# Kernel optimization log

Hardware: AMD Instinct MI355X
Metric: run time of the kernel (lower is better)

## Reference

```python
import jax, jax.numpy as jnp
import numpy as np
from jax import lax

IMG = 512            # image H = W
FH = FW = 32         # feature map spatial size
A = 9                # anchors per location (3 sizes x 3 ratios)
N = FH * FW * A      # total anchors = 9216
IOU_THR = 0.7
MIN_SCORE = 0.5
MIN_SIZE = 1e-3


def make_anchors():
    """Anchors in centroid format (cx, cy, w, h), ordered (H, W, A)."""
    stride = IMG / FH
    sizes = np.array([32.0, 64.0, 128.0])
    ratios = np.array([0.5, 1.0, 2.0])
    ws = (sizes[:, None] / np.sqrt(ratios)[None, :]).reshape(-1)  # (A,)
    hs = (sizes[:, None] * np.sqrt(ratios)[None, :]).reshape(-1)  # (A,)
    cx = (np.arange(FW) + 0.5) * stride
    cy = (np.arange(FH) + 0.5) * stride
    CX = np.broadcast_to(cx[None, :, None], (FH, FW, A))
    CY = np.broadcast_to(cy[:, None, None], (FH, FW, A))
    Wg = np.broadcast_to(ws[None, None, :], (FH, FW, A))
    Hg = np.broadcast_to(hs[None, None, :], (FH, FW, A))
    anc = np.stack([CX, CY, Wg, Hg], axis=-1).reshape(-1, 4)
    return jnp.asarray(anc, dtype=jnp.float32)


def pairwise_iou(b):
    # b: (N,4) corners x1,y1,x2,y2
    x1, y1, x2, y2 = b[:, 0], b[:, 1], b[:, 2], b[:, 3]
    area = (x2 - x1) * (y2 - y1)
    ix1 = jnp.maximum(x1[:, None], x1[None, :])
    iy1 = jnp.maximum(y1[:, None], y1[None, :])
    ix2 = jnp.minimum(x2[:, None], x2[None, :])
    iy2 = jnp.minimum(y2[:, None], y2[None, :])
    inter = jnp.maximum(ix2 - ix1, 0.0) * jnp.maximum(iy2 - iy1, 0.0)
    union = area[:, None] + area[None, :] - inter
    return inter / jnp.maximum(union, 1e-9)


def nms_keep(boxes, scores, valid):
    """Greedy NMS. Returns bool keep mask of shape (N,). Index decisions only."""
    s = jnp.where(valid, scores, -jnp.inf)
    order = jnp.argsort(-s)
    b = boxes[order]
    v = valid[order]
    ious = pairwise_iou(b)  # (N, N)
    idx = jnp.arange(N)

    def body(i, supp):
        keep_i = (~supp[i]) & v[i]
        return supp | (keep_i & (ious[i] > IOU_THR) & (idx > i))

    supp = lax.fori_loop(0, N, body, jnp.zeros(N, dtype=bool))
    keep_sorted = (~supp) & v
    return jnp.zeros(N, dtype=bool).at[order].set(keep_sorted)


def setup_inputs() -> dict:
    key = jax.random.key(0)
    ks = jax.random.split(key, 4)
    return {
        "feature_map": jax.random.normal(ks[0], (1, 256, FH, FW), jnp.float32),
        "conv1_w": jax.random.normal(ks[1], (512, 256, 3, 3), jnp.float32) * 0.02,
        "conv1_b": jnp.zeros((512,), jnp.float32),
        "conv2_w": jax.random.normal(ks[2], (A, 512), jnp.float32) * 0.01,
        "conv2_b": jnp.zeros((A,), jnp.float32),
        "conv3_w": jax.random.normal(ks[3], (4 * A, 512), jnp.float32) * 0.01,
        "conv3_b": jnp.zeros((4 * A,), jnp.float32),
    }


def reference(feature_map, conv1_w, conv1_b, conv2_w, conv2_b, conv3_w, conv3_b):
    anchors = make_anchors()  # (N,4) cx,cy,w,h

    # --- conv backbone head ---
    h = lax.conv_general_dilated(
        feature_map, conv1_w, (1, 1), "SAME",
        dimension_numbers=("NCHW", "OIHW", "NCHW"))
    h = jax.nn.relu(h + conv1_b[None, :, None, None])  # (1,512,H,W)

    scores = jax.nn.sigmoid(
        jnp.einsum("bchw,ac->bahw", h, conv2_w) + conv2_b[None, :, None, None])
    scores = scores.transpose(0, 2, 3, 1).reshape(-1)  # (N,) ordered (H,W,A)

    off = jnp.einsum("bchw,oc->bohw", h, conv3_w) + conv3_b[None, :, None, None]
    off = off.reshape(1, A, 4, FH, FW).transpose(0, 3, 4, 1, 2).reshape(-1, 4)

    acx, acy, aw, ah = anchors[:, 0], anchors[:, 1], anchors[:, 2], anchors[:, 3]
    cx = acx + off[:, 0] * aw
    cy = acy + off[:, 1] * ah
    bw = aw * jnp.exp(off[:, 2])
    bh = ah * jnp.exp(off[:, 3])
    boxes = jnp.stack([cx - bw / 2, cy - bh / 2, cx + bw / 2, cy + bh / 2], axis=1)

    # --- clip to image ---
    lo = jnp.array([0.0, 0.0, 0.0, 0.0], jnp.float32)
    hi = jnp.array([IMG, IMG, IMG, IMG], jnp.float32)
    boxes = jnp.clip(boxes, lo, hi)

    # --- remove small boxes + score threshold (as a mask, jit-safe) ---
    valid = ((boxes[:, 2] - boxes[:, 0]) >= MIN_SIZE) \
          & ((boxes[:, 3] - boxes[:, 1]) >= MIN_SIZE) \
          & (scores >= MIN_SCORE)

    # --- NMS (selection is index-based; no gradient through the decision) ---
    keep = nms_keep(lax.stop_gradient(boxes), lax.stop_gradient(scores), valid)

    out = jnp.concatenate(
        [boxes * keep[:, None].astype(boxes.dtype),
         (scores * keep.astype(scores.dtype))[:, None]], axis=1)  # (N,5)
    return out
```

## Files before the change

### kernel.cpp

```cpp
#include <hip/hip_runtime.h>
#include <math.h>

#define FHW   32
#define NA    9
#define NBOX  9216
#define C1    256
#define C2    512
#define KTOT  2304
#define KS    8
#define KCH   (KTOT / KS)
#define CAP   64
#define ECAP  16384
#define ROUNDS 96

struct AnchorWH { float w[NA]; float h[NA]; };

#define FP_OFF    0u
#define WT_OFF    1183744u
#define HP_OFF    5902336u
#define BOX_OFF   22679552u
#define SC_OFF    22827008u
#define VL_OFF    22863872u
#define DEG_OFF   22900736u
#define ADJ_OFF   22937600u
#define KEEP_OFF  24117248u
#define NV_OFF    24154112u

__global__ __launch_bounds__(256) void k_prep(const float* __restrict__ fin,
                                              float* __restrict__ Fp,
                                              unsigned int* __restrict__ deg,
                                              unsigned int* __restrict__ keepG,
                                              unsigned int* __restrict__ nv,
                                              const float* __restrict__ w1,
                                              float* __restrict__ Wt) {
    if (blockIdx.x < 1156) {
        int idx = blockIdx.x * 256 + threadIdx.x;
        if (idx < 256 * 34 * 34) {
            int c   = idx / 1156;
            int rem = idx - c * 1156;
            int yy  = rem / 34;
            int xx  = rem - yy * 34;
            float v = 0.f;
            if (yy >= 1 && yy <= 32 && xx >= 1 && xx <= 32)
                v = fin[c * 1024 + (yy - 1) * 32 + (xx - 1)];
            Fp[idx] = v;
        }
        if (idx < NBOX) { deg[idx] = 0u; keepG[idx] = 0u; }
        if (idx == 0)   *nv = 0u;
    } else {
        __shared__ float tile[32][33];
        int tb  = blockIdx.x - 1156;
        int k0  = (tb % 72) * 32;
        int oc0 = (tb / 72) * 32;
        int t   = threadIdx.x;
        int r0 = t >> 5, c = t & 31;
        #pragma unroll
        for (int i = 0; i < 4; ++i) {
            int r = r0 + 8 * i;
            tile[r][c] = w1[(oc0 + r) * KTOT + k0 + c];
        }
        __syncthreads();
        #pragma unroll
        for (int i = 0; i < 4; ++i) {
            int kk = r0 + 8 * i;
            Wt[(k0 + kk) * C2 + oc0 + c] = tile[c][kk];
        }
    }
}

__global__ __launch_bounds__(256, 2) void k_gemm(const float* __restrict__ Fp,
                                                 const float* __restrict__ Wt,
                                                 float* __restrict__ hp) {
    const int id = blockIdx.x;
    const int bx = id >> 5, g = id & 31;
    const int by = g >> 3, kz = g & 7;
    const int p0  = bx * 64;
    const int oc0 = by * 128;
    const int k0b = kz * KCH;
    const int t  = threadIdx.x;
    const int ty = t >> 4, tx = t & 15;

    __shared__ float As[16][64];
    __shared__ float Bs[16][128];

    float acc[4][8];
    #pragma unroll
    for (int r = 0; r < 4; ++r)
        #pragma unroll
        for (int c = 0; c < 8; ++c) acc[r][c] = 0.f;

    for (int kt = 0; kt < KCH; kt += 16) {
        #pragma unroll
        for (int i = 0; i < 4; ++i) {
            int e  = t + 256 * i;
            int kk = e >> 6, pp = e & 63;
            int k   = k0b + kt + kk;
            int c   = k / 9;
            int kap = k - c * 9;
            int dy  = kap / 3;
            int dx  = kap - dy * 3;
            int p  = p0 + pp;
            int y  = p >> 5, x = p & 31;
            As[kk][pp] = Fp[(c * 34 + y + dy) * 34 + x + dx];
        }
        #pragma unroll
        for (int i = 0; i < 2; ++i) {
            int e4 = t + 256 * i;
            int kk = e4 >> 5, c4 = e4 & 31;
            *(float4*)&Bs[kk][c4 * 4] =
                *(const float4*)&Wt[(k0b + kt + kk) * C2 + oc0 + c4 * 4];
        }
        __syncthreads();
        #pragma unroll
        for (int kk = 0; kk < 16; ++kk) {
            float a[4], b[8];
            *(float4*)&a[0] = *(const float4*)&As[kk][ty * 4];
            *(float4*)&b[0] = *(const float4*)&Bs[kk][tx * 4];
            *(float4*)&b[4] = *(const float4*)&Bs[kk][tx * 4 + 64];
            #pragma unroll
            for (int r = 0; r < 4; ++r)
                #pragma unroll
                for (int c = 0; c < 8; ++c) acc[r][c] += a[r] * b[c];
        }
        __syncthreads();
    }
    #pragma unroll
    for (int r = 0; r < 4; ++r) {
        int p = p0 + ty * 4 + r;
        float* dst = hp + ((kz * 1024 + p) * C2 + oc0 + tx * 4);
        *(float4*)dst        = *(float4*)&acc[r][0];
        *(float4*)(dst + 64) = *(float4*)&acc[r][4];
    }
}

__global__ __launch_bounds__(256) void k_heads(const float* __restrict__ hp,
                                               const float* __restrict__ b1,
                                               const float* __restrict__ w2,
                                               const float* __restrict__ b2,
                                               const float* __restrict__ w3,
                                               const float* __restrict__ b3,
                                               float* __restrict__ boxes,
                                               float* __restrict__ scoresG,
                                               unsigned int* __restrict__ nv,
                                               unsigned int* __restrict__ vlist,
                                               AnchorWH awh) {
    const int p0 = blockIdx.x * 4;
    const int t  = threadIdx.x;
    __shared__ float hrow[4][C2];
    __shared__ float arr[4][45];

    #pragma unroll
    for (int px = 0; px < 4; ++px) {
        int p = p0 + px;
        #pragma unroll
        for (int i = 0; i < 2; ++i) {
            int c = t + 256 * i;
            float s = b1[c];
            #pragma unroll
            for (int ks = 0; ks < KS; ++ks) s += hp[(ks * 1024 + p) * C2 + c];
            hrow[px][c] = fmaxf(s, 0.f);
        }
    }
    __syncthreads();

    const int w = t >> 6, lane = t & 63;
    for (int job = w; job < 180; job += 4) {
        int px = job / 45, j = job - px * 45;
        const float* wp = (j < 9) ? (w2 + j * C2) : (w3 + (j - 9) * C2);
        float s = 0.f;
        #pragma unroll
        for (int i = 0; i < 8; ++i) s += hrow[px][lane + 64 * i] * wp[lane + 64 * i];
        #pragma unroll
        for (int d = 1; d < 64; d <<= 1) s += __shfl_xor(s, d, 64);
        if (lane == 0) arr[px][j] = s;
    }
    __syncthreads();

    if (t < 36) {
        int px = t / 9, a = t - px * 9;
        int p = p0 + px;
        float logit = arr[px][a] + b2[a];
        float score = 1.f / (1.f + expf(-logit));
        float o0 = arr[px][9 + a * 4 + 0] + b3[a * 4 + 0];
        float o1 = arr[px][9 + a * 4 + 1] + b3[a * 4 + 1];
        float o2 = arr[px][9 + a * 4 + 2] + b3[a * 4 + 2];
        float o3 = arr[px][9 + a * 4 + 3] + b3[a * 4 + 3];
        int y = p >> 5, x = p & 31;
        float ax = (x + 0.5f) * 16.f, ay = (y + 0.5f) * 16.f;
        float aw = awh.w[a], ah = awh.h[a];
        float cx = ax + o0 * aw;
        float cy = ay + o1 * ah;
        float bw = aw * expf(o2);
        float bh = ah * expf(o3);
        float x1 = fminf(fmaxf(cx - bw * 0.5f, 0.f), 512.f);
        float y1 = fminf(fmaxf(cy - bh * 0.5f, 0.f), 512.f);
        float x2 = fminf(fmaxf(cx + bw * 0.5f, 0.f), 512.f);
        float y2 = fminf(fmaxf(cy + bh * 0.5f, 0.f), 512.f);
        int n = p * 9 + a;
        float4 bx4; bx4.x = x1; bx4.y = y1; bx4.z = x2; bx4.w = y2;
        ((float4*)boxes)[n] = bx4;
        scoresG[n] = score;
        bool valid = (x2 - x1 >= 0.001f) && (y2 - y1 >= 0.001f) && (score >= 0.5f);
        if (valid) {
            unsigned int ci = atomicAdd(nv, 1u);
            vlist[ci] = (unsigned int)n;
        }
    }
}

__global__ __launch_bounds__(256) void k_adj(const unsigned int* __restrict__ nvp,
                                             const unsigned int* __restrict__ vlist,
                                             const float* __restrict__ boxes,
                                             const float* __restrict__ scoresG,
                                             unsigned int* __restrict__ deg,
                                             unsigned short* __restrict__ adj) {
    const int Nv = (int)*nvp;
    int b = blockIdx.x;
    int tv = (int)(sqrtf(2.f * b + 0.25f) - 0.5f);
    while ((tv + 1) * (tv + 2) / 2 <= b) tv++;
    while (tv * (tv + 1) / 2 > b) tv--;
    int tu = b - tv * (tv + 1) / 2;
    if (tv * 128 >= Nv) return;

    __shared__ float4 ub[128], vb[128];
    __shared__ float  us[128], vs[128];
    __shared__ int    uo[128], vo[128];
    int t = threadIdx.x;
    if (t < 128) {
        int gi = tu * 128 + t;
        if (gi < Nv) { int n = (int)vlist[gi]; ub[t] = ((const float4*)boxes)[n]; us[t] = scoresG[n]; uo[t] = n; }
        else us[t] = -1.f;
    } else {
        int tt = t - 128;
        int gj = tv * 128 + tt;
        if (gj < Nv) { int n = (int)vlist[gj]; vb[tt] = ((const float4*)boxes)[n]; vs[tt] = scoresG[n]; vo[tt] = n; }
        else vs[tt] = -1.f;
    }
    __syncthreads();

    for (int s = 0; s < 64; ++s) {
        int q  = t + 256 * s;
        int i  = q >> 7, jj = q & 127;
        if (tu == tv && i >= jj) continue;
        float su = us[i], sv = vs[jj];
        if (su < 0.f || sv < 0.f) continue;
        float4 bu = ub[i], bv = vb[jj];
        float au = (bu.z - bu.x) * (bu.w - bu.y);
        float av = (bv.z - bv.x) * (bv.w - bv.y);
        float ix1 = fmaxf(bu.x, bv.x), iy1 = fmaxf(bu.y, bv.y);
        float ix2 = fminf(bu.z, bv.z), iy2 = fminf(bu.w, bv.w);
        float inter = fmaxf(ix2 - ix1, 0.f) * fmaxf(iy2 - iy1, 0.f);
        float uni = au + av - inter;
        float iou = inter / fmaxf(uni, 1e-9f);
        if (iou > 0.7f) {
            int gi = tu * 128 + i, gj = tv * 128 + jj;
            bool uHigh = (su > sv) || (su == sv && uo[i] < vo[jj]);
            int lower = uHigh ? gj : gi;
            int upper = uHigh ? gi : gj;
            unsigned int slot = atomicAdd(&deg[lower], 1u);
            if (slot < CAP) adj[lower * CAP + slot] = (unsigned short)upper;
        }
    }
}

__global__ __launch_bounds__(512) void k_peel(const unsigned int* __restrict__ nvp,
                                              const unsigned int* __restrict__ vlist,
                                              const unsigned int* __restrict__ degG,
                                              const unsigned short* __restrict__ adjG,
                                              unsigned int* __restrict__ keepG) {
    __shared__ unsigned short offL[NBOX + 2];
    __shared__ unsigned char  st[NBOX];
    __shared__ unsigned short csr[ECAP];
    __shared__ unsigned int   scratch[512];
    __shared__ unsigned char  flags[ROUNDS];
    const int t  = threadIdx.x;
    const int Nv = (int)*nvp;
    const int chunk = (Nv + 511) / 512;
    const int i0 = t * chunk;
    const int i1 = (i0 + chunk < Nv) ? (i0 + chunk) : Nv;

    if (t < ROUNDS) flags[t] = 0;

    unsigned int lsum = 0;
    for (int i = i0; i < i1; ++i) {
        unsigned int d = degG[i];
        if (d > CAP) d = CAP;
        st[i] = (unsigned char)d;
        lsum += d;
    }
    scratch[t] = lsum;
    __syncthreads();
    for (int ofs = 1; ofs < 512; ofs <<= 1) {
        unsigned int v = (t >= ofs) ? scratch[t - ofs] : 0u;
        __syncthreads();
        scratch[t] += v;
        __syncthreads();
    }
    if (t == 511) {
        unsigned int tot = scratch[511];
        offL[Nv] = (unsigned short)(tot < ECAP ? tot : ECAP);
    }
    unsigned int amask = 0;
    {
        unsigned int off = scratch[t] - lsum;
        for (int i = i0; i < i1; ++i) {
            unsigned int o = (off < ECAP) ? off : ECAP;
            offL[i] = (unsigned short)o;
            int d = st[i];
            int ld = (int)ECAP - (int)o; if (ld > d) ld = d; if (ld < 0) ld = 0;
            for (int s = 0; s < ld; ++s)
                csr[o + s] = adjG[i * CAP + s];
            off += d;
            if (d == 0) st[i] = 1;
            else { st[i] = 0; amask |= 1u << (i - i0); }
        }
    }
    __syncthreads();

    for (int r = 0; r < ROUNDS; ++r) {
        bool any = false;
        unsigned int m = amask;
        while (m) {
            int b = __ffs(m) - 1; m &= m - 1;
            int i = i0 + b;
            int o = offL[i], on = offL[i + 1];
            int d, ld;
            if (on < ECAP) { d = on - o; ld = d; }
            else {
                unsigned int dg = degG[i]; d = (dg > CAP) ? CAP : (int)dg;
                ld = (int)ECAP - o; if (ld < 0) ld = 0; if (ld > d) ld = d;
            }
            bool kseen = false, useen = false;
            for (int s = 0; s < d; ++s) {
                int j = (s < ld) ? (int)csr[o + s] : (int)adjG[i * CAP + s];
                unsigned char v = st[j];
                kseen |= (v == 1);
                useen |= (v == 0);
            }
            if (kseen)       { st[i] = 2; any = true; amask &= ~(1u << b); }
            else if (!useen) { st[i] = 1; any = true; amask &= ~(1u << b); }
        }
        if (any) flags[r] = 1;
        __syncthreads();
        if (!flags[r]) break;
    }

    for (int i = i0; i < i1; ++i)
        if (st[i] == 1) keepG[vlist[i]] = 1u;
}

__global__ __launch_bounds__(256) void k_out(const float* __restrict__ boxes,
                                             const float* __restrict__ scoresG,
                                             const unsigned int* __restrict__ keepG,
                                             float* __restrict__ out) {
    int n = blockIdx.x * 256 + threadIdx.x;
    if (n >= NBOX) return;
    float k = keepG[n] ? 1.f : 0.f;
    float4 b = ((const float4*)boxes)[n];
    out[n * 5 + 0] = b.x * k;
    out[n * 5 + 1] = b.y * k;
    out[n * 5 + 2] = b.z * k;
    out[n * 5 + 3] = b.w * k;
    out[n * 5 + 4] = scoresG[n] * k;
}

extern "C" void kernel_launch(void* const* d_in, const int* in_sizes, int n_in,
                              void* d_out, int out_size, void* d_ws, size_t ws_size,
                              hipStream_t stream) {
    const float* fin = (const float*)d_in[0];
    const float* w1  = (const float*)d_in[1];
    const float* b1  = (const float*)d_in[2];
    const float* w2  = (const float*)d_in[3];
    const float* b2  = (const float*)d_in[4];
    const float* w3  = (const float*)d_in[5];
    const float* b3  = (const float*)d_in[6];
    float* out = (float*)d_out;

    char* ws = (char*)d_ws;
    float*          Fp    = (float*)(ws + FP_OFF);
    float*          Wt    = (float*)(ws + WT_OFF);
    float*          hp    = (float*)(ws + HP_OFF);
    float*          boxes = (float*)(ws + BOX_OFF);
    float*          sc    = (float*)(ws + SC_OFF);
    unsigned int*   vlist = (unsigned int*)(ws + VL_OFF);
    unsigned int*   deg   = (unsigned int*)(ws + DEG_OFF);
    unsigned short* adj   = (unsigned short*)(ws + ADJ_OFF);
    unsigned int*   keepG = (unsigned int*)(ws + KEEP_OFF);
    unsigned int*   nv    = (unsigned int*)(ws + NV_OFF);

    AnchorWH awh;
    {
        const double sizes[3]  = {32.0, 64.0, 128.0};
        const double ratios[3] = {0.5, 1.0, 2.0};
        for (int si = 0; si < 3; ++si)
            for (int ri = 0; ri < 3; ++ri) {
                awh.w[si * 3 + ri] = (float)(sizes[si] / sqrt(ratios[ri]));
                awh.h[si * 3 + ri] = (float)(sizes[si] * sqrt(ratios[ri]));
            }
    }

    k_prep<<<dim3(1156 + 72 * 16), 256, 0, stream>>>(fin, Fp, deg, keepG, nv, w1, Wt);
    k_gemm<<<dim3(512), 256, 0, stream>>>(Fp, Wt, hp);
    k_heads<<<dim3(256), 256, 0, stream>>>(hp, b1, w2, b2, w3, b3, boxes, sc, nv, vlist, awh);
    k_adj<<<dim3(72 * 73 / 2), 256, 0, stream>>>(nv, vlist, boxes, sc, deg, adj);
    k_peel<<<dim3(1), 512, 0, stream>>>(nv, vlist, deg, adj, keepG);
    k_out<<<dim3((NBOX + 255) / 256), 256, 0, stream>>>(boxes, sc, keepG, out);
}
```

Measured before the change: 203.7 us.

## Add 16-way split-K GEMM with 8x8 register tiles and register prefetch

Adds a new conv-GEMM variant that splits K into 16 chunks, uses 128-thread blocks with 8x8 per-thread accumulators, and prefetches the next A/B tiles into registers while computing the current one. It is selected only when the workspace is large enough for 16 partial-sum slices. The workspace layout is reordered so the partial-sum buffer sits last, and the heads kernel takes the split count at runtime. The goal is more blocks and more latency hiding in the GEMM. The cost is twice the partial-sum write and read traffic in the heads reduction, plus higher register pressure.

```diff
diff --git a/kernel.cpp b/kernel.cpp
--- a/kernel.cpp
+++ b/kernel.cpp
@@ -7,8 +7,10 @@
 #define C1    256
 #define C2    512
 #define KTOT  2304
-#define KS    8
-#define KCH   (KTOT / KS)
+#define KS8   8
+#define KCH8  288
+#define KS16  16
+#define KCH16 144
 #define CAP   64
 #define ECAP  16384
 #define ROUNDS 96
@@ -17,14 +19,15 @@
 
 #define FP_OFF    0u
 #define WT_OFF    1183744u
-#define HP_OFF    5902336u
-#define BOX_OFF   22679552u
-#define SC_OFF    22827008u
-#define VL_OFF    22863872u
-#define DEG_OFF   22900736u
-#define ADJ_OFF   22937600u
-#define KEEP_OFF  24117248u
-#define NV_OFF    24154112u
+#define BOX_OFF   5902336u
+#define SC_OFF    6049792u
+#define VL_OFF    6086656u
+#define DEG_OFF   6123520u
+#define KEEP_OFF  6160384u
+#define NV_OFF    6197248u
+#define ADJ_OFF   6197504u
+#define HP_OFF    7377152u
+#define WS_NEED16 (HP_OFF + (size_t)KS16 * 1024 * 512 * 4)
 
 __global__ __launch_bounds__(256) void k_prep(const float* __restrict__ fin,
                                               float* __restrict__ Fp,
@@ -68,15 +71,111 @@
     }
 }
 
-__global__ __launch_bounds__(256, 2) void k_gemm(const float* __restrict__ Fp,
-                                                 const float* __restrict__ Wt,
-                                                 float* __restrict__ hp) {
+__global__ __launch_bounds__(128, 2) void k_gemm16(const float* __restrict__ Fp,
+                                                   const float* __restrict__ Wt,
+                                                   float* __restrict__ hp) {
+    const int id = blockIdx.x;
+    const int bx = id >> 6, g = id & 63;
+    const int by = g >> 4, kz = g & 15;
+    const int p0 = bx * 64, oc0 = by * 128, k0b = kz * KCH16;
+    const int t  = threadIdx.x;
+    const int ty = t >> 4, tx = t & 15;
+
+    __shared__ float As[16][64];
+    __shared__ float Bs[16][128];
+
+    float acc[8][8];
+    #pragma unroll
+    for (int r = 0; r < 8; ++r)
+        #pragma unroll
+        for (int c = 0; c < 8; ++c) acc[r][c] = 0.f;
+
+    float  pa[8];
+    float4 pb[4];
+
+    #pragma unroll
+    for (int i = 0; i < 8; ++i) {
+        int e = t + 128 * i;
+        int kk = e >> 6, pp = e & 63;
+        int k = k0b + kk;
+        int c = k / 9;
+        int kap = k - c * 9;
+        int dy = kap / 3, dx = kap - dy * 3;
+        int p = p0 + pp;
+        int y = p >> 5, x = p & 31;
+        pa[i] = Fp[(c * 34 + y + dy) * 34 + x + dx];
+    }
+    #pragma unroll
+    for (int i = 0; i < 4; ++i) {
+        int e4 = t + 128 * i;
+        int kk = e4 >> 5, c4 = e4 & 31;
+        pb[i] = *(const float4*)&Wt[(k0b + kk) * C2 + oc0 + c4 * 4];
+    }
+
+    for (int kt = 0; kt < KCH16; kt += 16) {
+        #pragma unroll
+        for (int i = 0; i < 8; ++i) {
+            int e = t + 128 * i;
+            As[e >> 6][e & 63] = pa[i];
+        }
+        #pragma unroll
+        for (int i = 0; i < 4; ++i) {
+            int e4 = t + 128 * i;
+            *(float4*)&Bs[e4 >> 5][(e4 & 31) * 4] = pb[i];
+        }
+        __syncthreads();
+        if (kt + 16 < KCH16) {
+            #pragma unroll
+            for (int i = 0; i < 8; ++i) {
+                int e = t + 128 * i;
+                int kk = e >> 6, pp = e & 63;
+                int k = k0b + kt + 16 + kk;
+                int c = k / 9;
+                int kap = k - c * 9;
+                int dy = kap / 3, dx = kap - dy * 3;
+                int p = p0 + pp;
+                int y = p >> 5, x = p & 31;
+                pa[i] = Fp[(c * 34 + y + dy) * 34 + x + dx];
+            }
+            #pragma unroll
+            for (int i = 0; i < 4; ++i) {
+                int e4 = t + 128 * i;
+                int kk = e4 >> 5, c4 = e4 & 31;
+                pb[i] = *(const float4*)&Wt[(k0b + kt + 16 + kk) * C2 + oc0 + c4 * 4];
+            }
+        }
+        #pragma unroll
+        for (int kk = 0; kk < 16; ++kk) {
+            float a[8], b[8];
+            *(float4*)&a[0] = *(const float4*)&As[kk][ty * 4];
+            *(float4*)&a[4] = *(const float4*)&As[kk][ty * 4 + 32];
+            *(float4*)&b[0] = *(const float4*)&Bs[kk][tx * 4];
+            *(float4*)&b[4] = *(const float4*)&Bs[kk][tx * 4 + 64];
+            #pragma unroll
+            for (int r = 0; r < 8; ++r)
+                #pragma unroll
+                for (int c = 0; c < 8; ++c) acc[r][c] += a[r] * b[c];
+        }
+        __syncthreads();
+    }
+    #pragma unroll
+    for (int r = 0; r < 8; ++r) {
+        int p = p0 + ty * 4 + (r & 3) + 32 * (r >> 2);
+        float* dst = hp + ((kz * 1024 + p) * C2 + oc0 + tx * 4);
+        *(float4*)dst        = *(float4*)&acc[r][0];
+        *(float4*)(dst + 64) = *(float4*)&acc[r][4];
+    }
+}
+
+__global__ __launch_bounds__(256, 2) void k_gemm8(const float* __restrict__ Fp,
+                                                  const float* __restrict__ Wt,
+                                                  float* __restrict__ hp) {
     const int id = blockIdx.x;
     const int bx = id >> 5, g = id & 31;
     const int by = g >> 3, kz = g & 7;
     const int p0  = bx * 64;
     const int oc0 = by * 128;
-    const int k0b = kz * KCH;
+    const int k0b = kz * KCH8;
     const int t  = threadIdx.x;
     const int ty = t >> 4, tx = t & 15;
 
@@ -89,7 +188,7 @@
         #pragma unroll
         for (int c = 0; c < 8; ++c) acc[r][c] = 0.f;
 
-    for (int kt = 0; kt < KCH; kt += 16) {
+    for (int kt = 0; kt < KCH8; kt += 16) {
         #pragma unroll
         for (int i = 0; i < 4; ++i) {
             int e  = t + 256 * i;
@@ -143,7 +242,7 @@
                                                float* __restrict__ scoresG,
                                                unsigned int* __restrict__ nv,
                                                unsigned int* __restrict__ vlist,
-                                               AnchorWH awh) {
+                                               AnchorWH awh, int KSdyn) {
     const int p0 = blockIdx.x * 4;
     const int t  = threadIdx.x;
     __shared__ float hrow[4][C2];
@@ -156,8 +255,8 @@
         for (int i = 0; i < 2; ++i) {
             int c = t + 256 * i;
             float s = b1[c];
-            #pragma unroll
-            for (int ks = 0; ks < KS; ++ks) s += hp[(ks * 1024 + p) * C2 + c];
+            #pragma unroll 4
+            for (int ks = 0; ks < KSdyn; ++ks) s += hp[(ks * 1024 + p) * C2 + c];
             hrow[px][c] = fmaxf(s, 0.f);
         }
     }
@@ -379,14 +478,17 @@
     char* ws = (char*)d_ws;
     float*          Fp    = (float*)(ws + FP_OFF);
     float*          Wt    = (float*)(ws + WT_OFF);
-    float*          hp    = (float*)(ws + HP_OFF);
     float*          boxes = (float*)(ws + BOX_OFF);
     float*          sc    = (float*)(ws + SC_OFF);
     unsigned int*   vlist = (unsigned int*)(ws + VL_OFF);
     unsigned int*   deg   = (unsigned int*)(ws + DEG_OFF);
-    unsigned short* adj   = (unsigned short*)(ws + ADJ_OFF);
     unsigned int*   keepG = (unsigned int*)(ws + KEEP_OFF);
     unsigned int*   nv    = (unsigned int*)(ws + NV_OFF);
+    unsigned short* adj   = (unsigned short*)(ws + ADJ_OFF);
+    float*          hp    = (float*)(ws + HP_OFF);
+
+    const bool big = (ws_size >= WS_NEED16);
+    const int  KSdyn = big ? KS16 : KS8;
 
     AnchorWH awh;
     {
@@ -400,8 +502,9 @@
     }
 
     k_prep<<<dim3(1156 + 72 * 16), 256, 0, stream>>>(fin, Fp, deg, keepG, nv, w1, Wt);
-    k_gemm<<<dim3(512), 256, 0, stream>>>(Fp, Wt, hp);
-    k_heads<<<dim3(256), 256, 0, stream>>>(hp, b1, w2, b2, w3, b3, boxes, sc, nv, vlist, awh);
+    if (big) k_gemm16<<<dim3(1024), 128, 0, stream>>>(Fp, Wt, hp);
+    else     k_gemm8 <<<dim3(512),  256, 0, stream>>>(Fp, Wt, hp);
+    k_heads<<<dim3(256), 256, 0, stream>>>(hp, b1, w2, b2, w3, b3, boxes, sc, nv, vlist, awh, KSdyn);
     k_adj<<<dim3(72 * 73 / 2), 256, 0, stream>>>(nv, vlist, boxes, sc, deg, adj);
     k_peel<<<dim3(1), 512, 0, stream>>>(nv, vlist, deg, adj, keepG);
     k_out<<<dim3((NBOX + 255) / 256), 256, 0, stream>>>(boxes, sc, keepG, out);
```

Result: slower. 226.0 us (+10.9%).

## Fuse all stages into one persistent kernel with software grid barriers

Applied to the files above, without the earlier changes.

Replaces six separate launches with a single persistent kernel of 512 blocks that moves between stages using an atomic-counter grid barrier. The heads stage now covers 2 pixels per block, the adjacency stage loops over dynamically sized tiles based on the valid count, and peel runs on block 0 with 256 threads and 64-bit active masks. The intent is to remove launch and inter-kernel gaps. In exchange it relies on all 512 blocks being co-resident, shrinks the shared CSR capacity, and the single-block peel stage now has half the threads.

```diff
diff --git a/kernel.cpp b/kernel.cpp
--- a/kernel.cpp
+++ b/kernel.cpp
@@ -8,360 +8,377 @@
 #define C2    512
 #define KTOT  2304
 #define KS    8
-#define KCH   (KTOT / KS)
+#define KCH   288
 #define CAP   64
-#define ECAP  16384
+#define ECAP  12288
 #define ROUNDS 96
+#define NBLK  512
 
 struct AnchorWH { float w[NA]; float h[NA]; };
 
 #define FP_OFF    0u
 #define WT_OFF    1183744u
-#define HP_OFF    5902336u
-#define BOX_OFF   22679552u
-#define SC_OFF    22827008u
-#define VL_OFF    22863872u
-#define DEG_OFF   22900736u
-#define ADJ_OFF   22937600u
-#define KEEP_OFF  24117248u
-#define NV_OFF    24154112u
-
-__global__ __launch_bounds__(256) void k_prep(const float* __restrict__ fin,
-                                              float* __restrict__ Fp,
-                                              unsigned int* __restrict__ deg,
-                                              unsigned int* __restrict__ keepG,
-                                              unsigned int* __restrict__ nv,
-                                              const float* __restrict__ w1,
-                                              float* __restrict__ Wt) {
-    if (blockIdx.x < 1156) {
-        int idx = blockIdx.x * 256 + threadIdx.x;
-        if (idx < 256 * 34 * 34) {
-            int c   = idx / 1156;
-            int rem = idx - c * 1156;
-            int yy  = rem / 34;
-            int xx  = rem - yy * 34;
-            float v = 0.f;
-            if (yy >= 1 && yy <= 32 && xx >= 1 && xx <= 32)
-                v = fin[c * 1024 + (yy - 1) * 32 + (xx - 1)];
-            Fp[idx] = v;
-        }
-        if (idx < NBOX) { deg[idx] = 0u; keepG[idx] = 0u; }
-        if (idx == 0)   *nv = 0u;
-    } else {
-        __shared__ float tile[32][33];
-        int tb  = blockIdx.x - 1156;
-        int k0  = (tb % 72) * 32;
-        int oc0 = (tb / 72) * 32;
-        int t   = threadIdx.x;
-        int r0 = t >> 5, c = t & 31;
+#define BOX_OFF   5902336u
+#define SC_OFF    6049792u
+#define VL_OFF    6086656u
+#define DEG_OFF   6123520u
+#define KEEP_OFF  6160384u
+#define NV_OFF    6197248u
+#define BAR_OFF   6197376u
+#define ADJ_OFF   6197504u
+#define HP_OFF    7377152u
+
+struct SmemPrep  { float tile[32][33]; };
+struct SmemGemm  { float As[16][64]; float Bs[16][128]; };
+struct SmemHeads { float hrow[2][C2]; float arr[2][45]; };
+struct SmemAdj   { float4 ub[128]; float4 vb[128]; float us[128]; float vs[128]; int uo[128]; int vo[128]; };
+struct SmemPeel  {
+    unsigned short offL[NBOX + 2];
+    unsigned char  st[NBOX];
+    unsigned short csr[ECAP];
+    unsigned int   scratch[256];
+    unsigned char  flags[ROUNDS];
+};
+union SmemU { SmemPrep p; SmemGemm g; SmemHeads h; SmemAdj a; SmemPeel e; };
+
+__device__ __forceinline__ void gbar(unsigned int* cnt, unsigned int phase) {
+    __syncthreads();
+    if (threadIdx.x == 0) {
+        __threadfence();
+        atomicAdd(cnt, 1u);
+        const unsigned int target = NBLK * phase;
+        while (atomicAdd(cnt, 0u) < target)
+            __builtin_amdgcn_s_sleep(15);
+        __threadfence();
+    }
+    __syncthreads();
+}
+
+__global__ __launch_bounds__(256, 2) void k_all(const float* __restrict__ fin,
+                                                const float* __restrict__ w1,
+                                                const float* __restrict__ b1,
+                                                const float* __restrict__ w2,
+                                                const float* __restrict__ b2,
+                                                const float* __restrict__ w3,
+                                                const float* __restrict__ b3,
+                                                float* __restrict__ out,
+                                                char* __restrict__ ws,
+                                                AnchorWH awh) {
+    __shared__ SmemU sm;
+
+    float*          Fp    = (float*)(ws + FP_OFF);
+    float*          Wt    = (float*)(ws + WT_OFF);
+    float*          boxes = (float*)(ws + BOX_OFF);
+    float*          sc    = (float*)(ws + SC_OFF);
+    unsigned int*   vlist = (unsigned int*)(ws + VL_OFF);
+    unsigned int*   deg   = (unsigned int*)(ws + DEG_OFF);
+    unsigned int*   keepG = (unsigned int*)(ws + KEEP_OFF);
+    unsigned int*   nvp   = (unsigned int*)(ws + NV_OFF);
+    unsigned int*   bar   = (unsigned int*)(ws + BAR_OFF);
+    unsigned short* adjG  = (unsigned short*)(ws + ADJ_OFF);
+    float*          hp    = (float*)(ws + HP_OFF);
+
+    const int t   = threadIdx.x;
+    const int gid = blockIdx.x * 256 + t;
+
+    for (int idx = gid; idx < 256 * 34 * 34; idx += NBLK * 256) {
+        int c   = idx / 1156;
+        int rem = idx - c * 1156;
+        int yy  = rem / 34;
+        int xx  = rem - yy * 34;
+        float v = 0.f;
+        if (yy >= 1 && yy <= 32 && xx >= 1 && xx <= 32)
+            v = fin[c * 1024 + (yy - 1) * 32 + (xx - 1)];
+        Fp[idx] = v;
+    }
+    if (gid < NBOX) { deg[gid] = 0u; keepG[gid] = 0u; }
+    if (gid == 0)   *nvp = 0u;
+    {
+        const int r0 = t >> 5, c = t & 31;
+        for (int tb = blockIdx.x; tb < 1152; tb += NBLK) {
+            int k0  = (tb % 72) * 32;
+            int oc0 = (tb / 72) * 32;
+            #pragma unroll
+            for (int i = 0; i < 4; ++i) {
+                int r = r0 + 8 * i;
+                sm.p.tile[r][c] = w1[(oc0 + r) * KTOT + k0 + c];
+            }
+            __syncthreads();
+            #pragma unroll
+            for (int i = 0; i < 4; ++i) {
+                int kk = r0 + 8 * i;
+                Wt[(k0 + kk) * C2 + oc0 + c] = sm.p.tile[c][kk];
+            }
+            __syncthreads();
+        }
+    }
+    gbar(bar, 1);
+
+    {
+        const int id = blockIdx.x;
+        const int bx = id >> 5, g = id & 31;
+        const int by = g >> 3, kz = g & 7;
+        const int p0  = bx * 64;
+        const int oc0 = by * 128;
+        const int k0b = kz * KCH;
+        const int ty = t >> 4, tx = t & 15;
+
+        float acc[4][8];
         #pragma unroll
-        for (int i = 0; i < 4; ++i) {
-            int r = r0 + 8 * i;
-            tile[r][c] = w1[(oc0 + r) * KTOT + k0 + c];
+        for (int r = 0; r < 4; ++r)
+            #pragma unroll
+            for (int c = 0; c < 8; ++c) acc[r][c] = 0.f;
+
+        for (int kt = 0; kt < KCH; kt += 16) {
+            #pragma unroll
+            for (int i = 0; i < 4; ++i) {
+                int e  = t + 256 * i;
+                int kk = e >> 6, pp = e & 63;
+                int k   = k0b + kt + kk;
+                int c   = k / 9;
+                int kap = k - c * 9;
+                int dy  = kap / 3;
+                int dx  = kap - dy * 3;
+                int p  = p0 + pp;
+                int y  = p >> 5, x = p & 31;
+                sm.g.As[kk][pp] = Fp[(c * 34 + y + dy) * 34 + x + dx];
+            }
+            #pragma unroll
+            for (int i = 0; i < 2; ++i) {
+                int e4 = t + 256 * i;
+                int kk = e4 >> 5, c4 = e4 & 31;
+                *(float4*)&sm.g.Bs[kk][c4 * 4] =
+                    *(const float4*)&Wt[(k0b + kt + kk) * C2 + oc0 + c4 * 4];
+            }
+            __syncthreads();
+            #pragma unroll
+            for (int kk = 0; kk < 16; ++kk) {
+                float a[4], b[8];
+                *(float4*)&a[0] = *(const float4*)&sm.g.As[kk][ty * 4];
+                *(float4*)&b[0] = *(const float4*)&sm.g.Bs[kk][tx * 4];
+                *(float4*)&b[4] = *(const float4*)&sm.g.Bs[kk][tx * 4 + 64];
+                #pragma unroll
+                for (int r = 0; r < 4; ++r)
+                    #pragma unroll
+                    for (int c = 0; c < 8; ++c) acc[r][c] += a[r] * b[c];
+            }
+            __syncthreads();
+        }
+        #pragma unroll
+        for (int r = 0; r < 4; ++r) {
+            int p = p0 + ty * 4 + r;
+            float* dst = hp + ((kz * 1024 + p) * C2 + oc0 + tx * 4);
+            *(float4*)dst        = *(float4*)&acc[r][0];
+            *(float4*)(dst + 64) = *(float4*)&acc[r][4];
+        }
+    }
+    gbar(bar, 2);
+
+    {
+        const int p0 = blockIdx.x * 2;
+        #pragma unroll
+        for (int px = 0; px < 2; ++px) {
+            int p = p0 + px;
+            #pragma unroll
+            for (int i = 0; i < 2; ++i) {
+                int c = t + 256 * i;
+                float s = b1[c];
+                #pragma unroll
+                for (int ks = 0; ks < KS; ++ks) s += hp[(ks * 1024 + p) * C2 + c];
+                sm.h.hrow[px][c] = fmaxf(s, 0.f);
+            }
         }
         __syncthreads();
-        #pragma unroll
-        for (int i = 0; i < 4; ++i) {
-            int kk = r0 + 8 * i;
-            Wt[(k0 + kk) * C2 + oc0 + c] = tile[c][kk];
-        }
-    }
-}
-
-__global__ __launch_bounds__(256, 2) void k_gemm(const float* __restrict__ Fp,
-                                                 const float* __restrict__ Wt,
-                                                 float* __restrict__ hp) {
-    const int id = blockIdx.x;
-    const int bx = id >> 5, g = id & 31;
-    const int by = g >> 3, kz = g & 7;
-    const int p0  = bx * 64;
-    const int oc0 = by * 128;
-    const int k0b = kz * KCH;
-    const int t  = threadIdx.x;
-    const int ty = t >> 4, tx = t & 15;
-
-    __shared__ float As[16][64];
-    __shared__ float Bs[16][128];
-
-    float acc[4][8];
-    #pragma unroll
-    for (int r = 0; r < 4; ++r)
-        #pragma unroll
-        for (int c = 0; c < 8; ++c) acc[r][c] = 0.f;
-
-    for (int kt = 0; kt < KCH; kt += 16) {
-        #pragma unroll
-        for (int i = 0; i < 4; ++i) {
-            int e  = t + 256 * i;
-            int kk = e >> 6, pp = e & 63;
-            int k   = k0b + kt + kk;
-            int c   = k / 9;
-            int kap = k - c * 9;
-            int dy  = kap / 3;
-            int dx  = kap - dy * 3;
-            int p  = p0 + pp;
-            int y  = p >> 5, x = p & 31;
-            As[kk][pp] = Fp[(c * 34 + y + dy) * 34 + x + dx];
-        }
-        #pragma unroll
-        for (int i = 0; i < 2; ++i) {
-            int e4 = t + 256 * i;
-            int kk = e4 >> 5, c4 = e4 & 31;
-            *(float4*)&Bs[kk][c4 * 4] =
-                *(const float4*)&Wt[(k0b + kt + kk) * C2 + oc0 + c4 * 4];
+
+        const int w = t >> 6, lane = t & 63;
+        for (int job = w; job < 90; job += 4) {
+            int px = job / 45, j = job - px * 45;
+            const float* wp = (j < 9) ? (w2 + j * C2) : (w3 + (j - 9) * C2);
+            float s = 0.f;
+            #pragma unroll
+            for (int i = 0; i < 8; ++i)
+                s += sm.h.hrow[px][lane + 64 * i] * wp[lane + 64 * i];
+            #pragma unroll
+            for (int d = 1; d < 64; d <<= 1) s += __shfl_xor(s, d, 64);
+            if (lane == 0) sm.h.arr[px][j] = s;
         }
         __syncthreads();
-        #pragma unroll
-        for (int kk = 0; kk < 16; ++kk) {
-            float a[4], b[8];
-            *(float4*)&a[0] = *(const float4*)&As[kk][ty * 4];
-            *(float4*)&b[0] = *(const float4*)&Bs[kk][tx * 4];
-            *(float4*)&b[4] = *(const float4*)&Bs[kk][tx * 4 + 64];
-            #pragma unroll
-            for (int r = 0; r < 4; ++r)
-                #pragma unroll
-                for (int c = 0; c < 8; ++c) acc[r][c] += a[r] * b[c];
-        }
+
+        if (t < 18) {
+            int px = t / 9, a = t - px * 9;
+            int p = p0 + px;
+            float logit = sm.h.arr[px][a] + b2[a];
+            float score = 1.f / (1.f + expf(-logit));
+            float o0 = sm.h.arr[px][9 + a * 4 + 0] + b3[a * 4 + 0];
+            float o1 = sm.h.arr[px][9 + a * 4 + 1] + b3[a * 4 + 1];
+            float o2 = sm.h.arr[px][9 + a * 4 + 2] + b3[a * 4 + 2];
+            float o3 = sm.h.arr[px][9 + a * 4 + 3] + b3[a * 4 + 3];
+            int y = p >> 5, x = p & 31;
+            float ax = (x + 0.5f) * 16.f, ay = (y + 0.5f) * 16.f;
+            float aw = awh.w[a], ah = awh.h[a];
+            float cx = ax + o0 * aw;
+            float cy = ay + o1 * ah;
+            float bw = aw * expf(o2);
+            float bh = ah * expf(o3);
+            float x1 = fminf(fmaxf(cx - bw * 0.5f, 0.f), 512.f);
+            float y1 = fminf(fmaxf(cy - bh * 0.5f, 0.f), 512.f);
+            float x2 = fminf(fmaxf(cx + bw * 0.5f, 0.f), 512.f);
+            float y2 = fminf(fmaxf(cy + bh * 0.5f, 0.f), 512.f);
+            int n = p * 9 + a;
+            float4 bx4; bx4.x = x1; bx4.y = y1; bx4.z = x2; bx4.w = y2;
+            ((float4*)boxes)[n] = bx4;
+            sc[n] = score;
+            bool valid = (x2 - x1 >= 0.001f) && (y2 - y1 >= 0.001f) && (score >= 0.5f);
+            if (valid) {
+                unsigned int ci = atomicAdd(nvp, 1u);
+                vlist[ci] = (unsigned int)n;
+            }
+        }
+    }
+    gbar(bar, 3);
+
+    {
+        const int Nv = (int)*nvp;
+        const int T  = (Nv + 127) / 128;
+        const int nTiles = T * (T + 1) / 2;
+        for (int b = blockIdx.x; b < nTiles; b += NBLK) {
+            int tv = (int)(sqrtf(2.f * b + 0.25f) - 0.5f);
+            while ((tv + 1) * (tv + 2) / 2 <= b) tv++;
+            while (tv * (tv + 1) / 2 > b) tv--;
+            int tu = b - tv * (tv + 1) / 2;
+
+            if (t < 128) {
+                int gi = tu * 128 + t;
+                if (gi < Nv) {
+                    int n = (int)vlist[gi];
+                    sm.a.ub[t] = ((const float4*)boxes)[n];
+                    sm.a.us[t] = sc[n]; sm.a.uo[t] = n;
+                } else sm.a.us[t] = -1.f;
+            } else {
+                int tt = t - 128;
+                int gj = tv * 128 + tt;
+                if (gj < Nv) {
+                    int n = (int)vlist[gj];
+                    sm.a.vb[tt] = ((const float4*)boxes)[n];
+                    sm.a.vs[tt] = sc[n]; sm.a.vo[tt] = n;
+                } else sm.a.vs[tt] = -1.f;
+            }
+            __syncthreads();
+
+            for (int s = 0; s < 64; ++s) {
+                int q  = t + 256 * s;
+                int i  = q >> 7, jj = q & 127;
+                if (tu == tv && i >= jj) continue;
+                float su = sm.a.us[i], sv = sm.a.vs[jj];
+                if (su < 0.f || sv < 0.f) continue;
+                float4 bu = sm.a.ub[i], bv = sm.a.vb[jj];
+                float au = (bu.z - bu.x) * (bu.w - bu.y);
+                float av = (bv.z - bv.x) * (bv.w - bv.y);
+                float ix1 = fmaxf(bu.x, bv.x), iy1 = fmaxf(bu.y, bv.y);
+                float ix2 = fminf(bu.z, bv.z), iy2 = fminf(bu.w, bv.w);
+                float inter = fmaxf(ix2 - ix1, 0.f) * fmaxf(iy2 - iy1, 0.f);
+                float uni = au + av - inter;
+                float iou = inter / fmaxf(uni, 1e-9f);
+                if (iou > 0.7f) {
+                    int gi = tu * 128 + i, gj = tv * 128 + jj;
+                    bool uHigh = (su > sv) || (su == sv && sm.a.uo[i] < sm.a.vo[jj]);
+                    int lower = uHigh ? gj : gi;
+                    int upper = uHigh ? gi : gj;
+                    unsigned int slot = atomicAdd(&deg[lower], 1u);
+                    if (slot < CAP) adjG[lower * CAP + slot] = (unsigned short)upper;
+                }
+            }
+            __syncthreads();
+        }
+    }
+    gbar(bar, 4);
+
+    if (blockIdx.x == 0) {
+        const int Nv = (int)*nvp;
+        const int chunk = (Nv + 255) / 256;
+        const int i0 = t * chunk;
+        const int i1 = (i0 + chunk < Nv) ? (i0 + chunk) : Nv;
+
+        if (t < ROUNDS) sm.e.flags[t] = 0;
+
+        unsigned int lsum = 0;
+        for (int i = i0; i < i1; ++i) {
+            unsigned int d = deg[i];
+            if (d > CAP) d = CAP;
+            sm.e.st[i] = (unsigned char)d;
+            lsum += d;
+        }
+        sm.e.scratch[t] = lsum;
         __syncthreads();
-    }
-    #pragma unroll
-    for (int r = 0; r < 4; ++r) {
-        int p = p0 + ty * 4 + r;
-        float* dst = hp + ((kz * 1024 + p) * C2 + oc0 + tx * 4);
-        *(float4*)dst        = *(float4*)&acc[r][0];
-        *(float4*)(dst + 64) = *(float4*)&acc[r][4];
-    }
-}
-
-__global__ __launch_bounds__(256) void k_heads(const float* __restrict__ hp,
-                                               const float* __restrict__ b1,
-                                               const float* __restrict__ w2,
-                                               const float* __restrict__ b2,
-                                               const float* __restrict__ w3,
-                                               const float* __restrict__ b3,
-                                               float* __restrict__ boxes,
-                                               float* __restrict__ scoresG,
-                                               unsigned int* __restrict__ nv,
-                                               unsigned int* __restrict__ vlist,
-                                               AnchorWH awh) {
-    const int p0 = blockIdx.x * 4;
-    const int t  = threadIdx.x;
-    __shared__ float hrow[4][C2];
-    __shared__ float arr[4][45];
-
-    #pragma unroll
-    for (int px = 0; px < 4; ++px) {
-        int p = p0 + px;
-        #pragma unroll
-        for (int i = 0; i < 2; ++i) {
-            int c = t + 256 * i;
-            float s = b1[c];
-            #pragma unroll
-            for (int ks = 0; ks < KS; ++ks) s += hp[(ks * 1024 + p) * C2 + c];
-            hrow[px][c] = fmaxf(s, 0.f);
-        }
-    }
-    __syncthreads();
-
-    const int w = t >> 6, lane = t & 63;
-    for (int job = w; job < 180; job += 4) {
-        int px = job / 45, j = job - px * 45;
-        const float* wp = (j < 9) ? (w2 + j * C2) : (w3 + (j - 9) * C2);
-        float s = 0.f;
-        #pragma unroll
-        for (int i = 0; i < 8; ++i) s += hrow[px][lane + 64 * i] * wp[lane + 64 * i];
-        #pragma unroll
-        for (int d = 1; d < 64; d <<= 1) s += __shfl_xor(s, d, 64);
-        if (lane == 0) arr[px][j] = s;
-    }
-    __syncthreads();
-
-    if (t < 36) {
-        int px = t / 9, a = t - px * 9;
-        int p = p0 + px;
-        float logit = arr[px][a] + b2[a];
-        float score = 1.f / (1.f + expf(-logit));
-        float o0 = arr[px][9 + a * 4 + 0] + b3[a * 4 + 0];
-        float o1 = arr[px][9 + a * 4 + 1] + b3[a * 4 + 1];
-        float o2 = arr[px][9 + a * 4 + 2] + b3[a * 4 + 2];
-        float o3 = arr[px][9 + a * 4 + 3] + b3[a * 4 + 3];
-        int y = p >> 5, x = p & 31;
-        float ax = (x + 0.5f) * 16.f, ay = (y + 0.5f) * 16.f;
-        float aw = awh.w[a], ah = awh.h[a];
-        float cx = ax + o0 * aw;
-        float cy = ay + o1 * ah;
-        float bw = aw * expf(o2);
-        float bh = ah * expf(o3);
-        float x1 = fminf(fmaxf(cx - bw * 0.5f, 0.f), 512.f);
-        float y1 = fminf(fmaxf(cy - bh * 0.5f, 0.f), 512.f);
-        float x2 = fminf(fmaxf(cx + bw * 0.5f, 0.f), 512.f);
-        float y2 = fminf(fmaxf(cy + bh * 0.5f, 0.f), 512.f);
-        int n = p * 9 + a;
-        float4 bx4; bx4.x = x1; bx4.y = y1; bx4.z = x2; bx4.w = y2;
-        ((float4*)boxes)[n] = bx4;
-        scoresG[n] = score;
-        bool valid = (x2 - x1 >= 0.001f) && (y2 - y1 >= 0.001f) && (score >= 0.5f);
-        if (valid) {
-            unsigned int ci = atomicAdd(nv, 1u);
-            vlist[ci] = (unsigned int)n;
-        }
-    }
-}
-
-__global__ __launch_bounds__(256) void k_adj(const unsigned int* __restrict__ nvp,
-                                             const unsigned int* __restrict__ vlist,
-                                             const float* __restrict__ boxes,
-                                             const float* __restrict__ scoresG,
-                                             unsigned int* __restrict__ deg,
-                                             unsigned short* __restrict__ adj) {
-    const int Nv = (int)*nvp;
-    int b = blockIdx.x;
-    int tv = (int)(sqrtf(2.f * b + 0.25f) - 0.5f);
-    while ((tv + 1) * (tv + 2) / 2 <= b) tv++;
-    while (tv * (tv + 1) / 2 > b) tv--;
-    int tu = b - tv * (tv + 1) / 2;
-    if (tv * 128 >= Nv) return;
-
-    __shared__ float4 ub[128], vb[128];
-    __shared__ float  us[128], vs[128];
-    __shared__ int    uo[128], vo[128];
-    int t = threadIdx.x;
-    if (t < 128) {
-        int gi = tu * 128 + t;
-        if (gi < Nv) { int n = (int)vlist[gi]; ub[t] = ((const float4*)boxes)[n]; us[t] = scoresG[n]; uo[t] = n; }
-        else us[t] = -1.f;
-    } else {
-        int tt = t - 128;
-        int gj = tv * 128 + tt;
-        if (gj < Nv) { int n = (int)vlist[gj]; vb[tt] = ((const float4*)boxes)[n]; vs[tt] = scoresG[n]; vo[tt] = n; }
-        else vs[tt] = -1.f;
-    }
-    __syncthreads();
-
-    for (int s = 0; s < 64; ++s) {
-        int q  = t + 256 * s;
-        int i  = q >> 7, jj = q & 127;
-        if (tu == tv && i >= jj) continue;
-        float su = us[i], sv = vs[jj];
-        if (su < 0.f || sv < 0.f) continue;
-        float4 bu = ub[i], bv = vb[jj];
-        float au = (bu.z - bu.x) * (bu.w - bu.y);
-        float av = (bv.z - bv.x) * (bv.w - bv.y);
-        float ix1 = fmaxf(bu.x, bv.x), iy1 = fmaxf(bu.y, bv.y);
-        float ix2 = fminf(bu.z, bv.z), iy2 = fminf(bu.w, bv.w);
-        float inter = fmaxf(ix2 - ix1, 0.f) * fmaxf(iy2 - iy1, 0.f);
-        float uni = au + av - inter;
-        float iou = inter / fmaxf(uni, 1e-9f);
-        if (iou > 0.7f) {
-            int gi = tu * 128 + i, gj = tv * 128 + jj;
-            bool uHigh = (su > sv) || (su == sv && uo[i] < vo[jj]);
-            int lower = uHigh ? gj : gi;
-            int upper = uHigh ? gi : gj;
-            unsigned int slot = atomicAdd(&deg[lower], 1u);
-            if (slot < CAP) adj[lower * CAP + slot] = (unsigned short)upper;
-        }
-    }
-}
-
-__global__ __launch_bounds__(512) void k_peel(const unsigned int* __restrict__ nvp,
-                                              const unsigned int* __restrict__ vlist,
-                                              const unsigned int* __restrict__ degG,
-                                              const unsigned short* __restrict__ adjG,
-                                              unsigned int* __restrict__ keepG) {
-    __shared__ unsigned short offL[NBOX + 2];
-    __shared__ unsigned char  st[NBOX];
-    __shared__ unsigned short csr[ECAP];
-    __shared__ unsigned int   scratch[512];
-    __shared__ unsigned char  flags[ROUNDS];
-    const int t  = threadIdx.x;
-    const int Nv = (int)*nvp;
-    const int chunk = (Nv + 511) / 512;
-    const int i0 = t * chunk;
-    const int i1 = (i0 + chunk < Nv) ? (i0 + chunk) : Nv;
-
-    if (t < ROUNDS) flags[t] = 0;
-
-    unsigned int lsum = 0;
-    for (int i = i0; i < i1; ++i) {
-        unsigned int d = degG[i];
-        if (d > CAP) d = CAP;
-        st[i] = (unsigned char)d;
-        lsum += d;
-    }
-    scratch[t] = lsum;
-    __syncthreads();
-    for (int ofs = 1; ofs < 512; ofs <<= 1) {
-        unsigned int v = (t >= ofs) ? scratch[t - ofs] : 0u;
+        for (int ofs = 1; ofs < 256; ofs <<= 1) {
+            unsigned int v = (t >= ofs) ? sm.e.scratch[t - ofs] : 0u;
+            __syncthreads();
+            sm.e.scratch[t] += v;
+            __syncthreads();
+        }
+        if (t == 255) {
+            unsigned int tot = sm.e.scratch[255];
+            sm.e.offL[Nv] = (unsigned short)(tot < ECAP ? tot : ECAP);
+        }
+        unsigned long long amask = 0ull;
+        {
+            unsigned int off = sm.e.scratch[t] - lsum;
+            for (int i = i0; i < i1; ++i) {
+                unsigned int o = (off < ECAP) ? off : ECAP;
+                sm.e.offL[i] = (unsigned short)o;
+                int d = sm.e.st[i];
+                int ld = (int)ECAP - (int)o; if (ld > d) ld = d; if (ld < 0) ld = 0;
+                for (int s = 0; s < ld; ++s)
+                    sm.e.csr[o + s] = adjG[i * CAP + s];
+                off += d;
+                if (d == 0) sm.e.st[i] = 1;
+                else { sm.e.st[i] = 0; amask |= 1ull << (i - i0); }
+            }
+        }
         __syncthreads();
-        scratch[t] += v;
-        __syncthreads();
-    }
-    if (t == 511) {
-        unsigned int tot = scratch[511];
-        offL[Nv] = (unsigned short)(tot < ECAP ? tot : ECAP);
-    }
-    unsigned int amask = 0;
-    {
-        unsigned int off = scratch[t] - lsum;
-        for (int i = i0; i < i1; ++i) {
-            unsigned int o = (off < ECAP) ? off : ECAP;
-            offL[i] = (unsigned short)o;
-            int d = st[i];
-            int ld = (int)ECAP - (int)o; if (ld > d) ld = d; if (ld < 0) ld = 0;
-            for (int s = 0; s < ld; ++s)
-                csr[o + s] = adjG[i * CAP + s];
-            off += d;
-            if (d == 0) st[i] = 1;
-            else { st[i] = 0; amask |= 1u << (i - i0); }
-        }
-    }
-    __syncthreads();
-
-    for (int r = 0; r < ROUNDS; ++r) {
-        bool any = false;
-        unsigned int m = amask;
-        while (m) {
-            int b = __ffs(m) - 1; m &= m - 1;
-            int i = i0 + b;
-            int o = offL[i], on = offL[i + 1];
-            int d, ld;
-            if (on < ECAP) { d = on - o; ld = d; }
-            else {
-                unsigned int dg = degG[i]; d = (dg > CAP) ? CAP : (int)dg;
-                ld = (int)ECAP - o; if (ld < 0) ld = 0; if (ld > d) ld = d;
-            }
-            bool kseen = false, useen = false;
-            for (int s = 0; s < d; ++s) {
-                int j = (s < ld) ? (int)csr[o + s] : (int)adjG[i * CAP + s];
-                unsigned char v = st[j];
-                kseen |= (v == 1);
-                useen |= (v == 0);
-            }
-            if (kseen)       { st[i] = 2; any = true; amask &= ~(1u << b); }
-            else if (!useen) { st[i] = 1; any = true; amask &= ~(1u << b); }
-        }
-        if (any) flags[r] = 1;
-        __syncthreads();
-        if (!flags[r]) break;
-    }
-
-    for (int i = i0; i < i1; ++i)
-        if (st[i] == 1) keepG[vlist[i]] = 1u;
-}
-
-__global__ __launch_bounds__(256) void k_out(const float* __restrict__ boxes,
-                                             const float* __restrict__ scoresG,
-                                             const unsigned int* __restrict__ keepG,
-                                             float* __restrict__ out) {
-    int n = blockIdx.x * 256 + threadIdx.x;
-    if (n >= NBOX) return;
-    float k = keepG[n] ? 1.f : 0.f;
-    float4 b = ((const float4*)boxes)[n];
-    out[n * 5 + 0] = b.x * k;
-    out[n * 5 + 1] = b.y * k;
-    out[n * 5 + 2] = b.z * k;
-    out[n * 5 + 3] = b.w * k;
-    out[n * 5 + 4] = scoresG[n] * k;
+
+        for (int r = 0; r < ROUNDS; ++r) {
+            bool any = false;
+            unsigned long long m = amask;
+            while (m) {
+                int b = __builtin_ctzll(m); m &= m - 1;
+                int i = i0 + b;
+                int o = sm.e.offL[i], on = sm.e.offL[i + 1];
+                int d, ld;
+                if (on < ECAP) { d = on - o; ld = d; }
+                else {
+                    unsigned int dg = deg[i]; d = (dg > CAP) ? CAP : (int)dg;
+                    ld = (int)ECAP - o; if (ld < 0) ld = 0; if (ld > d) ld = d;
+                }
+                bool kseen = false, useen = false;
+                for (int s = 0; s < d; ++s) {
+                    int j = (s < ld) ? (int)sm.e.csr[o + s] : (int)adjG[i * CAP + s];
+                    unsigned char v = sm.e.st[j];
+                    kseen |= (v == 1);
+                    useen |= (v == 0);
+                }
+                if (kseen)       { sm.e.st[i] = 2; any = true; amask &= ~(1ull << b); }
+                else if (!useen) { sm.e.st[i] = 1; any = true; amask &= ~(1ull << b); }
+            }
+            if (any) sm.e.flags[r] = 1;
+            __syncthreads();
+            if (!sm.e.flags[r]) break;
+        }
+
+        for (int i = i0; i < i1; ++i)
+            if (sm.e.st[i] == 1) keepG[vlist[i]] = 1u;
+    }
+    gbar(bar, 5);
+
+    if (gid < NBOX) {
+        float k = keepG[gid] ? 1.f : 0.f;
+        float4 b = ((const float4*)boxes)[gid];
+        out[gid * 5 + 0] = b.x * k;
+        out[gid * 5 + 1] = b.y * k;
+        out[gid * 5 + 2] = b.z * k;
+        out[gid * 5 + 3] = b.w * k;
+        out[gid * 5 + 4] = sc[gid] * k;
+    }
 }
 
 extern "C" void kernel_launch(void* const* d_in, const int* in_sizes, int n_in,
@@ -375,18 +392,7 @@
     const float* w3  = (const float*)d_in[5];
     const float* b3  = (const float*)d_in[6];
     float* out = (float*)d_out;
-
-    char* ws = (char*)d_ws;
-    float*          Fp    = (float*)(ws + FP_OFF);
-    float*          Wt    = (float*)(ws + WT_OFF);
-    float*          hp    = (float*)(ws + HP_OFF);
-    float*          boxes = (float*)(ws + BOX_OFF);
-    float*          sc    = (float*)(ws + SC_OFF);
-    unsigned int*   vlist = (unsigned int*)(ws + VL_OFF);
-    unsigned int*   deg   = (unsigned int*)(ws + DEG_OFF);
-    unsigned short* adj   = (unsigned short*)(ws + ADJ_OFF);
-    unsigned int*   keepG = (unsigned int*)(ws + KEEP_OFF);
-    unsigned int*   nv    = (unsigned int*)(ws + NV_OFF);
+    char*  ws  = (char*)d_ws;
 
     AnchorWH awh;
     {
@@ -399,10 +405,7 @@
             }
     }
 
-    k_prep<<<dim3(1156 + 72 * 16), 256, 0, stream>>>(fin, Fp, deg, keepG, nv, w1, Wt);
-    k_gemm<<<dim3(512), 256, 0, stream>>>(Fp, Wt, hp);
-    k_heads<<<dim3(256), 256, 0, stream>>>(hp, b1, w2, b2, w3, b3, boxes, sc, nv, vlist, awh);
-    k_adj<<<dim3(72 * 73 / 2), 256, 0, stream>>>(nv, vlist, boxes, sc, deg, adj);
-    k_peel<<<dim3(1), 512, 0, stream>>>(nv, vlist, deg, adj, keepG);
-    k_out<<<dim3((NBOX + 255) / 256), 256, 0, stream>>>(boxes, sc, keepG, out);
+    hipMemsetAsync(ws + BAR_OFF, 0, 64, stream);
+    k_all<<<dim3(NBLK), dim3(256), 0, stream>>>(fin, w1, b1, w2, b2, w3, b3,
+                                                out, ws, awh);
 }
```

New measurement: 407.3 us. 100.0% more time.
